# Performance work log

Hardware: AMD Instinct MI355X
Metric: run time of the kernel (lower is better)

Reference implementation:

```python
import jax, jax.numpy as jnp
import numpy as np

B, T, V, EMB, KBD, H, NF, OUT = 256, 50, 100000, 64, 64, 128, 10, 64


def setup_inputs() -> dict:
    key = jax.random.key(0)
    ks = jax.random.split(key, 18)
    s = 0.05
    f = lambda i, shape: jax.random.normal(ks[i], shape, jnp.float32) * s
    return {
        "X": jax.random.randint(ks[0], (B, T), 0, V),
        "E": f(1, (V, EMB)),
        "KBE": f(2, (V, KBD)),
        "r_matrix": f(3, (NF, KBD)),
        "gru_Wih": f(4, (3 * H, EMB)),
        "gru_Whh": f(5, (3 * H, H)),
        "gru_bih": f(6, (3 * H,)),
        "gru_bhh": f(7, (3 * H,)),
        "u_W": f(8, (KBD, H)),
        "u_b": f(9, (KBD,)),
        "ea_W": f(10, (KBD, KBD)),
        "ea_b": f(11, (KBD,)),
        "u2_W": f(12, (H, KBD + H)),
        "u2_b": f(13, (H,)),
        "m1_W": f(14, (OUT, H)),
        "m1_b": f(15, (OUT,)),
        "m2_W": f(16, (OUT, EMB + KBD)),
        "m2_b": f(17, (OUT,)),
    }


def reference(X, E, KBE, r_matrix, gru_Wih, gru_Whh, gru_bih, gru_bhh,
              u_W, u_b, ea_W, ea_b, u2_W, u2_b, m1_W, m1_b, m2_W, m2_b):
    b, t = X.shape
    nf, d = r_matrix.shape
    hdim = gru_Whh.shape[1]
    # mask row 0 of the embedding tables (padding item)
    Em = E.at[0].set(0.0)
    KBEm = KBE.at[0].set(0.0)
    Sx = Em[X]        # [B,T,EMB]
    KBx = KBEm[X]     # [B,T,KBD]

    h0 = jnp.zeros((b, hdim), Sx.dtype)
    MN0 = jnp.zeros((b, nf, d), Sx.dtype)
    ysum0 = jnp.zeros((b, m1_b.shape[0]), Sx.dtype)

    def step(carry, xs):
        h, MN, ysum = carry
        x_emb, kb = xs
        # torch GRUCell
        gi = x_emb @ gru_Wih.T + gru_bih
        gh = h @ gru_Whh.T + gru_bhh
        ir, iz, inn = jnp.split(gi, 3, axis=1)
        hr, hz, hn = jnp.split(gh, 3, axis=1)
        r = jax.nn.sigmoid(ir + hr)
        z = jax.nn.sigmoid(iz + hz)
        n = jnp.tanh(inn + r * hn)
        h = (1.0 - z) * n + z * h
        # memory write
        EA = jnp.tanh(kb @ ea_W.T + ea_b)[:, None, :] + r_matrix      # [B,NF,D]
        gate = jax.nn.sigmoid(jnp.sum(MN * EA, axis=-1, keepdims=True))  # [B,NF,1]
        MN = MN * (1.0 - gate) + EA * gate
        # memory read
        U = jnp.tanh(h @ u_W.T + u_b)                                  # [B,D]
        AW = jax.nn.softmax(U @ r_matrix.T, axis=1)                    # [B,NF]
        AC = jnp.einsum('bnd,bn->bd', MN, AW)                          # [B,D]
        Ut = jnp.tanh(jnp.concatenate([h, AC], axis=-1) @ u2_W.T + u2_b)
        y = jnp.tanh(Ut @ m1_W.T + m1_b)                               # [B,OUT]
        return (h, MN, ysum + y), None

    (h, MN, ysum), _ = jax.lax.scan(
        step, (h0, MN0, ysum0),
        (Sx.transpose(1, 0, 2), KBx.transpose(1, 0, 2)))
    y = ysum / t

    MergeE = jnp.concatenate([E, KBE], axis=1).at[0].set(0.0)  # [V, EMB+KBD]
    Sy = jnp.tanh(MergeE @ m2_W.T + m2_b)                      # [V, OUT]
    return jax.nn.log_softmax(y @ Sy.T, axis=1)                # [B, V]
```

## Files before the change

kernel.cpp:

```cpp
#include <hip/hip_runtime.h>
#include <hip/hip_bf16.h>
#include <math.h>

#define BB 256
#define TT 50
#define VV 100000
#define EMB 64
#define KBD 64
#define HH 128
#define NF 10
#define OUTD 64
#define G3H 384
#define NTILE 6250
#define DSTR 16
#define NSY 240

typedef __attribute__((ext_vector_type(8))) short sh8;
typedef __attribute__((ext_vector_type(4))) short sh4;
typedef __attribute__((ext_vector_type(4))) float f32x4;

__device__ __forceinline__ float frcp(float x){ return __builtin_amdgcn_rcpf(x); }
__device__ __forceinline__ float sigm(float x){ return frcp(1.0f+__expf(-x)); }
__device__ __forceinline__ float tanhf_(float x){ return 1.0f - 2.0f*frcp(__expf(2.0f*x)+1.0f); }
__device__ __forceinline__ short f2bs(float f){ __hip_bfloat16 h=__float2bfloat16(f); return *reinterpret_cast<short*>(&h); }
__device__ __forceinline__ sh8 ldfrag(const float* p){
  float4 a = *(const float4*)p; float4 b = *(const float4*)(p+4);
  sh8 v;
  v[0]=f2bs(a.x); v[1]=f2bs(a.y); v[2]=f2bs(a.z); v[3]=f2bs(a.w);
  v[4]=f2bs(b.x); v[5]=f2bs(b.y); v[6]=f2bs(b.z); v[7]=f2bs(b.w);
  return v;
}
__device__ __forceinline__ void barrier_lds(){
  asm volatile("s_waitcnt lgkmcnt(0)" ::: "memory");
  __builtin_amdgcn_sched_barrier(0);
  __builtin_amdgcn_s_barrier();
  __builtin_amdgcn_sched_barrier(0);
}

#define PREP 32
__global__ __launch_bounds__(512) void k_preSy(
    const int* __restrict__ X, const float* __restrict__ E, const float* __restrict__ KBE,
    const float* __restrict__ Wih, const float* __restrict__ bih, const float* __restrict__ bhh,
    const float* __restrict__ eaW, const float* __restrict__ eab,
    float* __restrict__ gi_pre, float* __restrict__ ea_pre,
    __hip_bfloat16* __restrict__ ea_bfT,
    const float* __restrict__ m2W, const float* __restrict__ m2b,
    __hip_bfloat16* __restrict__ Sy) {
  const int tid = threadIdx.x;
  const int w = tid>>6, l = tid&63, r16 = l&15, g4 = l>>4;

  if (blockIdx.x >= 400) {
    int kof = g4*8;
    sh8 bbf[4][4];
    float bias[4];
    #pragma unroll
    for (int nt=0;nt<4;nt++){
      int o = nt*16 + r16;
      bias[nt] = m2b[o];
      #pragma unroll
      for (int ks=0;ks<4;ks++) bbf[nt][ks] = ldfrag(m2W + o*128 + ks*32 + kof);
    }
    int wid = (blockIdx.x-400)*8 + w;
    for (int tile=wid; tile<NTILE; tile+=NSY*8){
      int v = tile*16 + r16;
      sh8 aa[4];
      const float* ep = E + (size_t)v*EMB + kof;
      const float* kp = KBE + (size_t)v*KBD + kof;
      aa[0] = ldfrag(ep); aa[1] = ldfrag(ep+32);
      aa[2] = ldfrag(kp); aa[3] = ldfrag(kp+32);
      if (v==0){ sh8 z={0,0,0,0,0,0,0,0}; aa[0]=z;aa[1]=z;aa[2]=z;aa[3]=z; }
      f32x4 acc[4];
      #pragma unroll
      for (int nt=0;nt<4;nt++){ f32x4 z={0.f,0.f,0.f,0.f}; acc[nt]=z; }
      #pragma unroll
      for (int nt=0;nt<4;nt++)
        #pragma unroll
        for (int ks=0;ks<4;ks++)
          acc[nt] = __builtin_amdgcn_mfma_f32_16x16x32_bf16(aa[ks],bbf[nt][ks],acc[nt],0,0,0);
      #pragma unroll
      for (int nt=0;nt<4;nt++){
        #pragma unroll
        for (int r=0;r<4;r++){
          int vv = tile*16 + g4*4 + r;
          Sy[(size_t)vv*OUTD + nt*16 + r16] = __float2bfloat16(tanhf_(acc[nt][r] + bias[nt]));
        }
      }
    }
    return;
  }

  __shared__ float xeL[PREP][68];
  __shared__ float kbL[PREP][68];
  int base = blockIdx.x * PREP;
  for (int i=tid; i<PREP*EMB; i+=512){
    int p=i>>6, k=i&63; int x = X[base+p];
    xeL[p][k] = x ? E[(size_t)x*EMB+k] : 0.0f;
    kbL[p][k] = x ? KBE[(size_t)x*KBD+k] : 0.0f;
  }
  __syncthreads();

  const int m = w>>2, nq = w&3;
  sh8 axe[2], akb[2];
  #pragma unroll
  for (int f=0;f<2;f++){
    axe[f] = ldfrag(&xeL[m*16 + r16][f*32 + g4*8]);
    akb[f] = ldfrag(&kbL[m*16 + r16][f*32 + g4*8]);
  }
  #pragma unroll
  for (int i=0;i<6;i++){
    int nt = nq*6 + i;
    int j = nt*16 + r16;
    sh8 bf0 = ldfrag(Wih + (size_t)j*EMB + g4*8);
    sh8 bf1 = ldfrag(Wih + (size_t)j*EMB + 32 + g4*8);
    f32x4 acc = {0.f,0.f,0.f,0.f};
    acc = __builtin_amdgcn_mfma_f32_16x16x32_bf16(axe[0], bf0, acc,0,0,0);
    acc = __builtin_amdgcn_mfma_f32_16x16x32_bf16(axe[1], bf1, acc,0,0,0);
    float bj = bih[j] + (j < 2*HH ? bhh[j] : 0.0f);
    #pragma unroll
    for (int r=0;r<4;r++){
      int pair = base + m*16 + g4*4 + r;
      gi_pre[(size_t)pair*G3H + j] = acc[r] + bj;
    }
  }
  {
    int d = nq*16 + r16;
    sh8 bf0 = ldfrag(eaW + (size_t)d*KBD + g4*8);
    sh8 bf1 = ldfrag(eaW + (size_t)d*KBD + 32 + g4*8);
    f32x4 acc = {0.f,0.f,0.f,0.f};
    acc = __builtin_amdgcn_mfma_f32_16x16x32_bf16(akb[0], bf0, acc,0,0,0);
    acc = __builtin_amdgcn_mfma_f32_16x16x32_bf16(akb[1], bf1, acc,0,0,0);
    float bd = eab[d];
    #pragma unroll
    for (int r=0;r<4;r++){
      int pair = base + m*16 + g4*4 + r;
      float v = tanhf(acc[r] + bd);
      ea_pre[(size_t)pair*KBD + d] = v;
      int bb = pair/TT, tt = pair - bb*TT;
      ea_bfT[((size_t)bb*64 + d)*64 + tt] = __float2bfloat16(v);
    }
  }
}

__global__ __launch_bounds__(256,2) void k_scanh(
    const float* __restrict__ gi_pre,
    const float* __restrict__ Whh, const float* __restrict__ bhh,
    const float* __restrict__ ea_pre, const float* __restrict__ rmat,
    float* __restrict__ Gg, float* __restrict__ Pg,
    __hip_bfloat16* __restrict__ h_stream) {
  const int tid = threadIdx.x;
  const int w = tid>>6, l = tid&63, r16 = l&15, g4 = l>>4;

  if (blockIdx.x >= 16) {
    const int b = (blockIdx.x-16)*4 + w;
    sh8 aa[4][2];
    #pragma unroll
    for (int i=0;i<4;i++){
      int row = i*16 + r16; if (row > TT-1) row = TT-1;
      #pragma unroll
      for (int f=0;f<2;f++)
        aa[i][f] = ldfrag(ea_pre + ((size_t)b*TT + row)*KBD + f*32 + g4*8);
    }
    sh8 rmB[2];
    #pragma unroll
    for (int f=0;f<2;f++){
      sh8 z = {0,0,0,0,0,0,0,0};
      if (r16 < NF) z = ldfrag(rmat + (size_t)r16*KBD + f*32 + g4*8);
      rmB[f] = z;
    }
    float* Gb = Gg + ((size_t)b<<12);
    #pragma unroll
    for (int i=0;i<4;i++){
      #pragma unroll
      for (int j=0;j<4;j++){
        f32x4 acc={0.f,0.f,0.f,0.f};
        #pragma unroll
        for (int f=0;f<2;f++) acc = __builtin_amdgcn_mfma_f32_16x16x32_bf16(aa[i][f], aa[j][f], acc,0,0,0);
        #pragma unroll
        for (int r=0;r<4;r++) Gb[(i*16+g4*4+r)*64 + j*16+r16] = acc[r];
      }
      f32x4 accp={0.f,0.f,0.f,0.f};
      #pragma unroll
      for (int f=0;f<2;f++) accp = __builtin_amdgcn_mfma_f32_16x16x32_bf16(aa[i][f], rmB[f], accp,0,0,0);
      #pragma unroll
      for (int r=0;r<4;r++) Pg[((size_t)b<<10) + (i*16+g4*4+r)*16 + r16] = accp[r];
    }
    return;
  }

  __shared__ __hip_bfloat16 hcat[2][16][128];
  __builtin_amdgcn_s_setprio(1);
  const int b = blockIdx.x;
  const int b0 = b*16;
  for (int i=tid;i<2*16*128;i+=256) ((short*)hcat)[i]=0;
  __syncthreads();
  const int swz = (r16&7)<<4;

  sh8 whhF[2][3][4];
  #pragma unroll
  for (int t=0;t<2;t++)
    #pragma unroll
    for (int g=0;g<3;g++){
      int chain = (w + 4*t) + 8*g;
      #pragma unroll
      for (int f=0;f<4;f++)
        whhF[t][g][f] = ldfrag(Whh + (size_t)(chain*16 + r16)*HH + f*32 + g4*8);
    }
  float4 bhn[2];
  bhn[0] = *(const float4*)(bhh + 2*HH + w*16 + g4*4);
  bhn[1] = *(const float4*)(bhh + 2*HH + (w+4)*16 + g4*4);
  float h_old[2][4] = {{0.f,0.f,0.f,0.f},{0.f,0.f,0.f,0.f}};
  const float* gi_row = gi_pre + (size_t)(b0+r16)*TT*G3H;
  __hip_bfloat16* hsb = h_stream + (size_t)b*TT*16*HH;

  int cur = 0;
  auto stepfn = [&](int s, float4 (&gi)[2][3], int cu){
    const char* hrow = (const char*)&hcat[cu][r16][0];
    sh8 hb[4];
    #pragma unroll
    for (int f=0;f<4;f++)
      hb[f] = *(const sh8*)(hrow + ((f*64 + g4*16) ^ swz));
    f32x4 aR[2], aZ[2], aN[2];
    #pragma unroll
    for (int t=0;t<2;t++){ f32x4 z={0.f,0.f,0.f,0.f}; aR[t]=z; aZ[t]=z; aN[t]=z; }
    #pragma unroll
    for (int f=0;f<4;f++){
      #pragma unroll
      for (int t=0;t<2;t++){
        aR[t] = __builtin_amdgcn_mfma_f32_16x16x32_bf16(whhF[t][0][f], hb[f], aR[t],0,0,0);
        aZ[t] = __builtin_amdgcn_mfma_f32_16x16x32_bf16(whhF[t][1][f], hb[f], aZ[t],0,0,0);
        aN[t] = __builtin_amdgcn_mfma_f32_16x16x32_bf16(whhF[t][2][f], hb[f], aN[t],0,0,0);
      }
    }
    char* hwrow = (char*)&hcat[cu^1][r16][0];
    #pragma unroll
    for (int t=0;t<2;t++){
      sh4 hp;
      #pragma unroll
      for (int r=0;r<4;r++){
        float rr = sigm(gi[t][0][r] + aR[t][r]);
        float zz = sigm(gi[t][1][r] + aZ[t][r]);
        float nn = tanhf_(gi[t][2][r] + rr*(aN[t][r] + bhn[t][r]));
        h_old[t][r] = (1.f-zz)*nn + zz*h_old[t][r];
        hp[r] = f2bs(h_old[t][r]);
      }
      *(sh4*)(hwrow + (((w+4*t)*32 + g4*8) ^ swz)) = hp;
      *(sh4*)(hsb + ((size_t)s*16 + r16)*HH + (w+4*t)*16 + g4*4) = hp;
    }
    barrier_lds();
  };

  float4 gA[2][3], gB[2][3];
  #pragma unroll
  for (int t=0;t<2;t++)
    #pragma unroll
    for (int g=0;g<3;g++)
      gA[t][g] = *(const float4*)(gi_row + g*128 + (w+4*t)*16 + g4*4);

  for (int s=0;s<TT;s+=2){
    {
      int sg = s+1;
      #pragma unroll
      for (int t=0;t<2;t++)
        #pragma unroll
        for (int g=0;g<3;g++)
          gB[t][g] = *(const float4*)(gi_row + (size_t)sg*G3H + g*128 + (w+4*t)*16 + g4*4);
      stepfn(s, gA, cur);
      cur ^= 1;
    }
    {
      int sg = (s+2<TT)? s+2 : TT-1;
      #pragma unroll
      for (int t=0;t<2;t++)
        #pragma unroll
        for (int g=0;g<3;g++)
          gA[t][g] = *(const float4*)(gi_row + (size_t)sg*G3H + g*128 + (w+4*t)*16 + g4*4);
      stepfn(s+1, gB, cur);
      cur ^= 1;
    }
  }
}

__global__ __launch_bounds__(512) void k_uaw(
    const __hip_bfloat16* __restrict__ h_stream,
    const float* __restrict__ uW, const float* __restrict__ ub,
    const float* __restrict__ rmat, float* __restrict__ aw_pre) {
  __shared__ __hip_bfloat16 u_sh[8][16][72];
  const int tid = threadIdx.x;
  const int w = tid>>6, l = tid&63, r16 = l&15, g4 = l>>4;
  sh8 uwF[4][4];
  #pragma unroll
  for (int ot=0;ot<4;ot++)
    #pragma unroll
    for (int f=0;f<4;f++)
      uwF[ot][f] = ldfrag(uW + (size_t)(ot*16+r16)*HH + f*32 + g4*8);
  sh8 rmF[2];
  #pragma unroll
  for (int f=0;f<2;f++){
    sh8 z = {0,0,0,0,0,0,0,0};
    if (r16 < NF) z = ldfrag(rmat + (size_t)r16*KBD + f*32 + g4*8);
    rmF[f] = z;
  }
  float4 ubv[4];
  #pragma unroll
  for (int ot=0;ot<4;ot++) ubv[ot] = *(const float4*)(ub + ot*16 + g4*4);

  int p0 = (blockIdx.x*8 + w)*16;
  int t = p0>>8, b0 = p0&255, fb = b0>>4;
  const __hip_bfloat16* hp = h_stream + (size_t)((fb*TT + t)*16)*HH;
  sh8 hb[4];
  #pragma unroll
  for (int f=0;f<4;f++) hb[f] = *(const sh8*)(hp + r16*HH + f*32 + g4*8);
  f32x4 u[4];
  #pragma unroll
  for (int ot=0;ot<4;ot++){ f32x4 z={0.f,0.f,0.f,0.f}; u[ot]=z; }
  #pragma unroll
  for (int ot=0;ot<4;ot++)
    #pragma unroll
    for (int f=0;f<4;f++)
      u[ot] = __builtin_amdgcn_mfma_f32_16x16x32_bf16(uwF[ot][f], hb[f], u[ot],0,0,0);
  #pragma unroll
  for (int ot=0;ot<4;ot++){
    sh4 up;
    #pragma unroll
    for (int r=0;r<4;r++) up[r] = f2bs(tanhf_(u[ot][r] + ubv[ot][r]));
    *(sh4*)&u_sh[w][l&15][ot*16 + g4*4] = up;
  }
  __syncthreads();
  sh8 uf[2];
  #pragma unroll
  for (int f=0;f<2;f++) uf[f] = *(const sh8*)&u_sh[w][r16][f*32 + g4*8];
  f32x4 al={0.f,0.f,0.f,0.f};
  #pragma unroll
  for (int f=0;f<2;f++) al = __builtin_amdgcn_mfma_f32_16x16x32_bf16(rmF[f], uf[f], al,0,0,0);
  float mx = -1e30f;
  #pragma unroll
  for (int r=0;r<4;r++){ if (g4*4+r < NF) mx = fmaxf(mx, al[r]); }
  mx = fmaxf(mx, __shfl_xor(mx,16));
  mx = fmaxf(mx, __shfl_xor(mx,32));
  float av[4]; float ssum=0.f;
  #pragma unroll
  for (int r=0;r<4;r++){ av[r] = (g4*4+r < NF) ? __expf(al[r]-mx) : 0.f; ssum += av[r]; }
  ssum += __shfl_xor(ssum,16); ssum += __shfl_xor(ssum,32);
  float inv = frcp(ssum);
  if (g4<3){
    f32x4 o = {av[0]*inv, av[1]*inv, av[2]*inv, av[3]*inv};
    *(f32x4*)&aw_pre[(size_t)(p0+r16)*16 + g4*4] = o;
  }
}

__global__ __launch_bounds__(640) void k_mnrec(
    const float* __restrict__ Gg, const float* __restrict__ Pg,
    const float* __restrict__ rmat, const float* __restrict__ aw_pre,
    __hip_bfloat16* __restrict__ Aag_bf, __hip_bfloat16* __restrict__ Bag_bf) {
  __shared__ float AagL[TT*52];
  __shared__ float BagL[TT*16];
  const int tid = threadIdx.x;
  const int n = tid>>6, l = tid&63;
  const int b = blockIdx.x;
  for (int i=tid;i<TT*52;i+=640) AagL[i]=0.f;
  for (int i=tid;i<TT*16;i+=640) BagL[i]=0.f;

  float rv = rmat[n*KBD + l];
  float R = rv*rv;
  R += __shfl_xor(R,1); R += __shfl_xor(R,2); R += __shfl_xor(R,4);
  R += __shfl_xor(R,8); R += __shfl_xor(R,16); R += __shfl_xor(R,32);

  float Pn = (l<TT)? Pg[((size_t)b<<10) + l*16 + n] : 0.f;
  const float* Gb = Gg + ((size_t)b<<12);
  float Grow = Gb[l];
  float awt = aw_pre[(size_t)(0*256+b)*16 + n];
  float d=0.f, w=0.f, q=1.f;
  __syncthreads();

  for (int t=0;t<TT;t++){
    int tn = (t+1<TT)? t+1 : TT-1;
    float GrowN = Gb[tn*64 + l];
    float awtN  = aw_pre[(size_t)(tn*256+b)*16 + n];
    float dt = __shfl(d, t);
    float g  = sigm(dt);
    float og = 1.f - g;
    float Pt = __shfl(Pn, t);
    float Ets = Grow + Pt + Pn + R;
    d = og*d + g*Ets;
    w = (l==t)? g : w*og;
    q *= og;
    if (l < TT) atomicAdd(&AagL[t*52 + l], awt*w);
    if (l == 0) BagL[t*16 + n] = awt*(1.f - q);
    Grow = GrowN; awt = awtN;
  }
  __syncthreads();
  for (int i=tid;i<4096;i+=640){
    int row=i>>6, col=i&63;
    float v = (row<TT && col<TT)? AagL[row*52+col] : 0.f;
    Aag_bf[((size_t)b<<12) + i] = __float2bfloat16(v);
  }
  for (int i=tid;i<2048;i+=640){
    int row=i>>5, col=i&31;
    float v = (row<TT && col<NF)? BagL[row*16+col] : 0.f;
    Bag_bf[((size_t)b<<11) + i] = __float2bfloat16(v);
  }
}

__global__ __launch_bounds__(512) void k_ac(
    const __hip_bfloat16* __restrict__ Aag_bf, const __hip_bfloat16* __restrict__ Bag_bf,
    const __hip_bfloat16* __restrict__ ea_bfT, const float* __restrict__ rmat,
    __hip_bfloat16* __restrict__ ac_pre) {
  const int tid = threadIdx.x;
  const int w = tid>>6, l = tid&63, r16 = l&15, g4 = l>>4;
  const int b = blockIdx.x*8 + w;
  sh8 a1[4][2], a2[4];
  #pragma unroll
  for (int i=0;i<4;i++){
    #pragma unroll
    for (int f=0;f<2;f++)
      a1[i][f] = *(const sh8*)(Aag_bf + ((size_t)b<<12) + (i*16+r16)*64 + f*32 + g4*8);
    a2[i] = *(const sh8*)(Bag_bf + ((size_t)b<<11) + (i*16+r16)*32 + g4*8);
  }
  for (int j=0;j<4;j++){
    sh8 bb1[2];
    #pragma unroll
    for (int f=0;f<2;f++)
      bb1[f] = *(const sh8*)(ea_bfT + ((size_t)b<<12) + (j*16+r16)*64 + f*32 + g4*8);
    sh8 bb2;
    #pragma unroll
    for (int c=0;c<8;c++){
      int k = g4*8 + c;
      bb2[c] = (k<NF)? f2bs(rmat[k*KBD + j*16+r16]) : (short)0;
    }
    #pragma unroll
    for (int i=0;i<4;i++){
      f32x4 acc={0.f,0.f,0.f,0.f};
      #pragma unroll
      for (int f=0;f<2;f++) acc = __builtin_amdgcn_mfma_f32_16x16x32_bf16(a1[i][f], bb1[f], acc,0,0,0);
      acc = __builtin_amdgcn_mfma_f32_16x16x32_bf16(a2[i], bb2, acc,0,0,0);
      #pragma unroll
      for (int r=0;r<4;r++){
        int t = i*16 + g4*4 + r;
        if (t < TT)
          ac_pre[((size_t)t*256 + b)*KBD + j*16 + r16] = __float2bfloat16(acc[r]);
      }
    }
  }
}

__global__ __launch_bounds__(512) void k_uty(
    const __hip_bfloat16* __restrict__ h_stream, const __hip_bfloat16* __restrict__ ac_pre,
    const float* __restrict__ u2W, const float* __restrict__ u2b,
    const float* __restrict__ m1W, const float* __restrict__ m1b,
    __hip_bfloat16* __restrict__ y_tmp) {
  __shared__ __hip_bfloat16 ut_sh[16][136];
  const int tid = threadIdx.x;
  const int w = tid>>6, l = tid&63, r16 = l&15, g4 = l>>4;
  const int t = blockIdx.x>>4, btile = blockIdx.x&15;
  const int b0 = btile*16, fb = btile;

  sh8 u2F[6];
  #pragma unroll
  for (int f=0;f<6;f++) u2F[f] = ldfrag(u2W + (size_t)(w*16+r16)*(HH+KBD) + f*32 + g4*8);
  sh8 m1F[4];
  if (w<4){
    #pragma unroll
    for (int f=0;f<4;f++) m1F[f] = ldfrag(m1W + (size_t)(w*16+r16)*HH + f*32 + g4*8);
  }
  float4 u2bv = *(const float4*)(u2b + w*16 + g4*4);

  const __hip_bfloat16* hp = h_stream + (size_t)((fb*TT + t)*16)*HH;
  const __hip_bfloat16* ap = ac_pre + ((size_t)t*256 + b0)*KBD;
  sh8 cb[6];
  #pragma unroll
  for (int f=0;f<4;f++) cb[f] = *(const sh8*)(hp + r16*HH + f*32 + g4*8);
  #pragma unroll
  for (int f=4;f<6;f++) cb[f] = *(const sh8*)(ap + r16*KBD + (f-4)*32 + g4*8);
  f32x4 at={0.f,0.f,0.f,0.f};
  #pragma unroll
  for (int f=0;f<6;f++) at = __builtin_amdgcn_mfma_f32_16x16x32_bf16(u2F[f], cb[f], at,0,0,0);
  sh4 tp;
  #pragma unroll
  for (int r=0;r<4;r++) tp[r] = f2bs(tanhf_(at[r] + u2bv[r]));
  *(sh4*)&ut_sh[r16][w*16+g4*4] = tp;
  __syncthreads();
  if (w<4){
    float4 m1bv = *(const float4*)(m1b + w*16 + g4*4);
    sh8 tb[4];
    #pragma unroll
    for (int f=0;f<4;f++) tb[f] = *(const sh8*)&ut_sh[r16][f*32+g4*8];
    f32x4 ay={0.f,0.f,0.f,0.f};
    #pragma unroll
    for (int f=0;f<4;f++) ay = __builtin_amdgcn_mfma_f32_16x16x32_bf16(m1F[f], tb[f], ay,0,0,0);
    sh4 yp;
    #pragma unroll
    for (int r=0;r<4;r++) yp[r] = f2bs(tanhf_(ay[r] + m1bv[r]));
    *(sh4*)&y_tmp[((size_t)t*256 + b0 + r16)*OUTD + w*16 + g4*4] = yp;
  }
}

__global__ __launch_bounds__(512) void k_fin(
    const __hip_bfloat16* __restrict__ y_tmp, __hip_bfloat16* __restrict__ ybf) {
  int idx = blockIdx.x*512 + threadIdx.x;
  int b = idx>>6, o = idx&63;
  float s = 0.f;
  for (int t=0;t<TT;t++) s += __bfloat162float(y_tmp[((size_t)t*256 + b)*OUTD + o]);
  ybf[(size_t)b*OUTD + o] = __float2bfloat16(s*(1.0f/TT));
}

__global__ __launch_bounds__(256) void k_logits(
    const __hip_bfloat16* __restrict__ ybf, const __hip_bfloat16* __restrict__ Sy,
    float* __restrict__ denom, float* __restrict__ out, int pass) {
  __shared__ float dsum[64];
  int lane = threadIdx.x & 63;
  int w = threadIdx.x >> 6;
  int r16 = lane & 15, g4 = lane >> 4;
  int kof = g4 * 8;
  int tbase = blockIdx.x * 16 + w * 4;
  if (pass==0){
    if (threadIdx.x<64) dsum[threadIdx.x]=0.f;
    __syncthreads();
  }
  sh8 b0[4], b1[4];
  #pragma unroll
  for (int i=0;i<4;i++){
    if (tbase + i < NTILE) {
      const __hip_bfloat16* bp = Sy + ((size_t)((tbase+i)*16 + r16))*OUTD + kof;
      b0[i] = *(const sh8*)bp;
      b1[i] = *(const sh8*)(bp + 32);
    } else {
      sh8 z = {0,0,0,0,0,0,0,0};
      b0[i]=z; b1[i]=z;
    }
  }
  int bg0 = blockIdx.y * 4;
  for (int bgi=0; bgi<4; bgi++){
    int bg = bg0 + bgi;
    const __hip_bfloat16* ap = ybf + (bg*16 + r16)*OUTD + kof;
    sh8 a0 = *(const sh8*)ap;
    sh8 a1 = *(const sh8*)(ap+32);
    if (pass == 0){
      float part[4] = {0.f,0.f,0.f,0.f};
      #pragma unroll
      for (int i=0;i<4;i++){
        if (tbase + i < NTILE){
          f32x4 acc = {0.f,0.f,0.f,0.f};
          acc = __builtin_amdgcn_mfma_f32_16x16x32_bf16(a0,b0[i],acc,0,0,0);
          acc = __builtin_amdgcn_mfma_f32_16x16x32_bf16(a1,b1[i],acc,0,0,0);
          #pragma unroll
          for (int r=0;r<4;r++) part[r] += __expf(acc[r]);
        }
      }
      #pragma unroll
      for (int r=0;r<4;r++){
        float p = part[r];
        p += __shfl_xor(p,1,16); p += __shfl_xor(p,2,16);
        p += __shfl_xor(p,4,16); p += __shfl_xor(p,8,16);
        if (r16==0) atomicAdd(&dsum[bgi*16 + g4*4 + r], p);
      }
    } else {
      float lse[4];
      #pragma unroll
      for (int r=0;r<4;r++) lse[r] = logf(denom[(size_t)(bg*16 + g4*4 + r)*DSTR]);
      #pragma unroll
      for (int i=0;i<4;i++){
        if (tbase + i < NTILE){
          f32x4 acc = {0.f,0.f,0.f,0.f};
          acc = __builtin_amdgcn_mfma_f32_16x16x32_bf16(a0,b0[i],acc,0,0,0);
          acc = __builtin_amdgcn_mfma_f32_16x16x32_bf16(a1,b1[i],acc,0,0,0);
          int vc = (tbase+i)*16 + r16;
          #pragma unroll
          for (int r=0;r<4;r++)
            out[(size_t)(bg*16 + g4*4 + r)*VV + vc] = acc[r] - lse[r];
        }
      }
    }
  }
  if (pass==0){
    __syncthreads();
    if (threadIdx.x<64)
      atomicAdd(&denom[(size_t)(bg0*16 + threadIdx.x)*DSTR], dsum[threadIdx.x]);
  }
}

extern "C" void kernel_launch(void* const* d_in, const int* in_sizes, int n_in,
                              void* d_out, int out_size, void* d_ws, size_t ws_size,
                              hipStream_t stream) {
  const int*   X    = (const int*)  d_in[0];
  const float* E    = (const float*)d_in[1];
  const float* KBE  = (const float*)d_in[2];
  const float* rmat = (const float*)d_in[3];
  const float* Wih  = (const float*)d_in[4];
  const float* Whh  = (const float*)d_in[5];
  const float* bih  = (const float*)d_in[6];
  const float* bhh  = (const float*)d_in[7];
  const float* uW   = (const float*)d_in[8];
  const float* ub   = (const float*)d_in[9];
  const float* eaW  = (const float*)d_in[10];
  const float* eab  = (const float*)d_in[11];
  const float* u2W  = (const float*)d_in[12];
  const float* u2b  = (const float*)d_in[13];
  const float* m1W  = (const float*)d_in[14];
  const float* m1b  = (const float*)d_in[15];
  const float* m2W  = (const float*)d_in[16];
  const float* m2b  = (const float*)d_in[17];
  float* outp = (float*)d_out;

  char* p = (char*)d_ws;
  float* gi_pre = (float*)p;            p += (size_t)BB*TT*G3H*4;
  float* ea_pre = (float*)p;            p += (size_t)BB*TT*KBD*4;
  float* denom  = (float*)p;            p += (size_t)BB*DSTR*4;
  float* aw_pre = (float*)p;            p += (size_t)BB*TT*16*4;
  float* Gg     = (float*)p;            p += (size_t)BB*64*64*4;
  float* Pg     = (float*)p;            p += (size_t)BB*64*16*4;
  __hip_bfloat16* h_stream = (__hip_bfloat16*)p; p += (size_t)16*TT*16*HH*2;
  __hip_bfloat16* ea_bfT = (__hip_bfloat16*)p;   p += (size_t)BB*64*64*2;
  __hip_bfloat16* Aag_bf = (__hip_bfloat16*)p;   p += (size_t)BB*64*64*2;
  __hip_bfloat16* Bag_bf = (__hip_bfloat16*)p;   p += (size_t)BB*64*32*2;
  __hip_bfloat16* ac_pre = (__hip_bfloat16*)p;   p += (size_t)BB*TT*KBD*2;
  __hip_bfloat16* y_tmp  = (__hip_bfloat16*)p;   p += (size_t)BB*TT*OUTD*2;
  __hip_bfloat16* ybf    = (__hip_bfloat16*)p;   p += (size_t)BB*OUTD*2;
  __hip_bfloat16* Sy     = (__hip_bfloat16*)p;   p += (size_t)VV*OUTD*2;

  hipMemsetAsync(denom, 0, BB*DSTR*sizeof(float), stream);
  k_preSy<<<400+NSY,512,0,stream>>>(X,E,KBE,Wih,bih,bhh,eaW,eab,gi_pre,ea_pre,ea_bfT,
                                    m2W,m2b,Sy);
  k_scanh<<<80,256,0,stream>>>(gi_pre,Whh,bhh,ea_pre,rmat,Gg,Pg,h_stream);
  k_uaw<<<100,512,0,stream>>>(h_stream,uW,ub,rmat,aw_pre);
  k_mnrec<<<256,640,0,stream>>>(Gg,Pg,rmat,aw_pre,Aag_bf,Bag_bf);
  k_ac<<<32,512,0,stream>>>(Aag_bf,Bag_bf,ea_bfT,rmat,ac_pre);
  k_uty<<<TT*16,512,0,stream>>>(h_stream,ac_pre,u2W,u2b,m1W,m1b,y_tmp);
  k_fin<<<32,512,0,stream>>>(y_tmp,ybf);
  dim3 g1((NTILE + 15)/16, 4, 1);
  k_logits<<<g1,256,0,stream>>>(ybf,Sy,denom,outp,0);
  k_logits<<<g1,256,0,stream>>>(ybf,Sy,denom,outp,1);
}
```

Measured before the change: 240.4 us.

## Fuse memory recurrence with AC matmul and move Sy computation into k_uty

Result: faster. 227.9 us (-5.2%).

```diff
diff --git a/kernel.cpp b/kernel.cpp
--- a/kernel.cpp
+++ b/kernel.cpp
@@ -38,57 +38,18 @@
 }
 
 #define PREP 32
-__global__ __launch_bounds__(512) void k_preSy(
+__global__ __launch_bounds__(512) void k_pre(
     const int* __restrict__ X, const float* __restrict__ E, const float* __restrict__ KBE,
     const float* __restrict__ Wih, const float* __restrict__ bih, const float* __restrict__ bhh,
     const float* __restrict__ eaW, const float* __restrict__ eab,
     float* __restrict__ gi_pre, float* __restrict__ ea_pre,
-    __hip_bfloat16* __restrict__ ea_bfT,
-    const float* __restrict__ m2W, const float* __restrict__ m2b,
-    __hip_bfloat16* __restrict__ Sy) {
+    __hip_bfloat16* __restrict__ ea_bfT, float* __restrict__ denom) {
   const int tid = threadIdx.x;
   const int w = tid>>6, l = tid&63, r16 = l&15, g4 = l>>4;
 
-  if (blockIdx.x >= 400) {
-    int kof = g4*8;
-    sh8 bbf[4][4];
-    float bias[4];
-    #pragma unroll
-    for (int nt=0;nt<4;nt++){
-      int o = nt*16 + r16;
-      bias[nt] = m2b[o];
-      #pragma unroll
-      for (int ks=0;ks<4;ks++) bbf[nt][ks] = ldfrag(m2W + o*128 + ks*32 + kof);
-    }
-    int wid = (blockIdx.x-400)*8 + w;
-    for (int tile=wid; tile<NTILE; tile+=NSY*8){
-      int v = tile*16 + r16;
-      sh8 aa[4];
-      const float* ep = E + (size_t)v*EMB + kof;
-      const float* kp = KBE + (size_t)v*KBD + kof;
-      aa[0] = ldfrag(ep); aa[1] = ldfrag(ep+32);
-      aa[2] = ldfrag(kp); aa[3] = ldfrag(kp+32);
-      if (v==0){ sh8 z={0,0,0,0,0,0,0,0}; aa[0]=z;aa[1]=z;aa[2]=z;aa[3]=z; }
-      f32x4 acc[4];
-      #pragma unroll
-      for (int nt=0;nt<4;nt++){ f32x4 z={0.f,0.f,0.f,0.f}; acc[nt]=z; }
-      #pragma unroll
-      for (int nt=0;nt<4;nt++)
-        #pragma unroll
-        for (int ks=0;ks<4;ks++)
-          acc[nt] = __builtin_amdgcn_mfma_f32_16x16x32_bf16(aa[ks],bbf[nt][ks],acc[nt],0,0,0);
-      #pragma unroll
-      for (int nt=0;nt<4;nt++){
-        #pragma unroll
-        for (int r=0;r<4;r++){
-          int vv = tile*16 + g4*4 + r;
-          Sy[(size_t)vv*OUTD + nt*16 + r16] = __float2bfloat16(tanhf_(acc[nt][r] + bias[nt]));
-        }
-      }
-    }
-    return;
-  }
-
+  if (blockIdx.x == 0){
+    for (int i=tid;i<BB*DSTR;i+=512) denom[i]=0.f;
+  }
   __shared__ float xeL[PREP][68];
   __shared__ float kbL[PREP][68];
   int base = blockIdx.x * PREP;
@@ -348,17 +309,18 @@
   }
 }
 
-__global__ __launch_bounds__(640) void k_mnrec(
+__global__ __launch_bounds__(640) void k_mnac(
     const float* __restrict__ Gg, const float* __restrict__ Pg,
     const float* __restrict__ rmat, const float* __restrict__ aw_pre,
-    __hip_bfloat16* __restrict__ Aag_bf, __hip_bfloat16* __restrict__ Bag_bf) {
-  __shared__ float AagL[TT*52];
-  __shared__ float BagL[TT*16];
+    const __hip_bfloat16* __restrict__ ea_bfT,
+    __hip_bfloat16* __restrict__ ac_pre) {
+  __shared__ float AagL[64*52];
+  __shared__ float BagL[64*16];
   const int tid = threadIdx.x;
   const int n = tid>>6, l = tid&63;
   const int b = blockIdx.x;
-  for (int i=tid;i<TT*52;i+=640) AagL[i]=0.f;
-  for (int i=tid;i<TT*16;i+=640) BagL[i]=0.f;
+  for (int i=tid;i<64*52;i+=640) AagL[i]=0.f;
+  for (int i=tid;i<64*16;i+=640) BagL[i]=0.f;
 
   float rv = rmat[n*KBD + l];
   float R = rv*rv;
@@ -369,7 +331,7 @@
   const float* Gb = Gg + ((size_t)b<<12);
   float Grow = Gb[l];
   float awt = aw_pre[(size_t)(0*256+b)*16 + n];
-  float d=0.f, w=0.f, q=1.f;
+  float d=0.f, w_=0.f, q=1.f;
   __syncthreads();
 
   for (int t=0;t<TT;t++){
@@ -382,41 +344,26 @@
     float Pt = __shfl(Pn, t);
     float Ets = Grow + Pt + Pn + R;
     d = og*d + g*Ets;
-    w = (l==t)? g : w*og;
+    w_ = (l==t)? g : w_*og;
     q *= og;
-    if (l < TT) atomicAdd(&AagL[t*52 + l], awt*w);
+    if (l < TT) atomicAdd(&AagL[t*52 + l], awt*w_);
     if (l == 0) BagL[t*16 + n] = awt*(1.f - q);
     Grow = GrowN; awt = awtN;
   }
   __syncthreads();
-  for (int i=tid;i<4096;i+=640){
-    int row=i>>6, col=i&63;
-    float v = (row<TT && col<TT)? AagL[row*52+col] : 0.f;
-    Aag_bf[((size_t)b<<12) + i] = __float2bfloat16(v);
-  }
-  for (int i=tid;i<2048;i+=640){
-    int row=i>>5, col=i&31;
-    float v = (row<TT && col<NF)? BagL[row*16+col] : 0.f;
-    Bag_bf[((size_t)b<<11) + i] = __float2bfloat16(v);
-  }
-}
-
-__global__ __launch_bounds__(512) void k_ac(
-    const __hip_bfloat16* __restrict__ Aag_bf, const __hip_bfloat16* __restrict__ Bag_bf,
-    const __hip_bfloat16* __restrict__ ea_bfT, const float* __restrict__ rmat,
-    __hip_bfloat16* __restrict__ ac_pre) {
-  const int tid = threadIdx.x;
-  const int w = tid>>6, l = tid&63, r16 = l&15, g4 = l>>4;
-  const int b = blockIdx.x*8 + w;
-  sh8 a1[4][2], a2[4];
-  #pragma unroll
-  for (int i=0;i<4;i++){
-    #pragma unroll
-    for (int f=0;f<2;f++)
-      a1[i][f] = *(const sh8*)(Aag_bf + ((size_t)b<<12) + (i*16+r16)*64 + f*32 + g4*8);
-    a2[i] = *(const sh8*)(Bag_bf + ((size_t)b<<11) + (i*16+r16)*32 + g4*8);
-  }
-  for (int j=0;j<4;j++){
+
+  const int w = n, r16 = l&15, g4 = l>>4;
+  if (w < 4){
+    sh8 a1[4][2], a2[4];
+    #pragma unroll
+    for (int i=0;i<4;i++){
+      int row = i*16 + r16;
+      #pragma unroll
+      for (int f=0;f<2;f++) a1[i][f] = ldfrag(&AagL[row*52 + f*32 + g4*8]);
+      a2[i] = ldfrag(&BagL[row*16 + ((g4*8) & 15)]);
+      if (g4 >= 2){ sh8 z={0,0,0,0,0,0,0,0}; a2[i]=z; }
+    }
+    int j = w;
     sh8 bb1[2];
     #pragma unroll
     for (int f=0;f<2;f++)
@@ -447,10 +394,54 @@
     const __hip_bfloat16* __restrict__ h_stream, const __hip_bfloat16* __restrict__ ac_pre,
     const float* __restrict__ u2W, const float* __restrict__ u2b,
     const float* __restrict__ m1W, const float* __restrict__ m1b,
-    __hip_bfloat16* __restrict__ y_tmp) {
+    __hip_bfloat16* __restrict__ y_tmp,
+    const float* __restrict__ E, const float* __restrict__ KBE,
+    const float* __restrict__ m2W, const float* __restrict__ m2b,
+    __hip_bfloat16* __restrict__ Sy) {
   __shared__ __hip_bfloat16 ut_sh[16][136];
   const int tid = threadIdx.x;
   const int w = tid>>6, l = tid&63, r16 = l&15, g4 = l>>4;
+
+  if (blockIdx.x >= 800) {
+    int kof = g4*8;
+    sh8 bbf[4][4];
+    float bias[4];
+    #pragma unroll
+    for (int nt=0;nt<4;nt++){
+      int o = nt*16 + r16;
+      bias[nt] = m2b[o];
+      #pragma unroll
+      for (int ks=0;ks<4;ks++) bbf[nt][ks] = ldfrag(m2W + o*128 + ks*32 + kof);
+    }
+    int wid = (blockIdx.x-800)*8 + w;
+    for (int tile=wid; tile<NTILE; tile+=NSY*8){
+      int v = tile*16 + r16;
+      sh8 aa[4];
+      const float* ep = E + (size_t)v*EMB + kof;
+      const float* kp = KBE + (size_t)v*KBD + kof;
+      aa[0] = ldfrag(ep); aa[1] = ldfrag(ep+32);
+      aa[2] = ldfrag(kp); aa[3] = ldfrag(kp+32);
+      if (v==0){ sh8 z={0,0,0,0,0,0,0,0}; aa[0]=z;aa[1]=z;aa[2]=z;aa[3]=z; }
+      f32x4 acc[4];
+      #pragma unroll
+      for (int nt=0;nt<4;nt++){ f32x4 z={0.f,0.f,0.f,0.f}; acc[nt]=z; }
+      #pragma unroll
+      for (int nt=0;nt<4;nt++)
+        #pragma unroll
+        for (int ks=0;ks<4;ks++)
+          acc[nt] = __builtin_amdgcn_mfma_f32_16x16x32_bf16(aa[ks],bbf[nt][ks],acc[nt],0,0,0);
+      #pragma unroll
+      for (int nt=0;nt<4;nt++){
+        #pragma unroll
+        for (int r=0;r<4;r++){
+          int vv = tile*16 + g4*4 + r;
+          Sy[(size_t)vv*OUTD + nt*16 + r16] = __float2bfloat16(tanhf_(acc[nt][r] + bias[nt]));
+        }
+      }
+    }
+    return;
+  }
+
   const int t = blockIdx.x>>4, btile = blockIdx.x&15;
   const int b0 = btile*16, fb = btile;
 
@@ -610,21 +601,17 @@
   float* Pg     = (float*)p;            p += (size_t)BB*64*16*4;
   __hip_bfloat16* h_stream = (__hip_bfloat16*)p; p += (size_t)16*TT*16*HH*2;
   __hip_bfloat16* ea_bfT = (__hip_bfloat16*)p;   p += (size_t)BB*64*64*2;
-  __hip_bfloat16* Aag_bf = (__hip_bfloat16*)p;   p += (size_t)BB*64*64*2;
-  __hip_bfloat16* Bag_bf = (__hip_bfloat16*)p;   p += (size_t)BB*64*32*2;
   __hip_bfloat16* ac_pre = (__hip_bfloat16*)p;   p += (size_t)BB*TT*KBD*2;
   __hip_bfloat16* y_tmp  = (__hip_bfloat16*)p;   p += (size_t)BB*TT*OUTD*2;
   __hip_bfloat16* ybf    = (__hip_bfloat16*)p;   p += (size_t)BB*OUTD*2;
   __hip_bfloat16* Sy     = (__hip_bfloat16*)p;   p += (size_t)VV*OUTD*2;
 
-  hipMemsetAsync(denom, 0, BB*DSTR*sizeof(float), stream);
-  k_preSy<<<400+NSY,512,0,stream>>>(X,E,KBE,Wih,bih,bhh,eaW,eab,gi_pre,ea_pre,ea_bfT,
-                                    m2W,m2b,Sy);
+  k_pre<<<400,512,0,stream>>>(X,E,KBE,Wih,bih,bhh,eaW,eab,gi_pre,ea_pre,ea_bfT,denom);
   k_scanh<<<80,256,0,stream>>>(gi_pre,Whh,bhh,ea_pre,rmat,Gg,Pg,h_stream);
   k_uaw<<<100,512,0,stream>>>(h_stream,uW,ub,rmat,aw_pre);
-  k_mnrec<<<256,640,0,stream>>>(Gg,Pg,rmat,aw_pre,Aag_bf,Bag_bf);
-  k_ac<<<32,512,0,stream>>>(Aag_bf,Bag_bf,ea_bfT,rmat,ac_pre);
-  k_uty<<<TT*16,512,0,stream>>>(h_stream,ac_pre,u2W,u2b,m1W,m1b,y_tmp);
+  k_mnac<<<256,640,0,stream>>>(Gg,Pg,rmat,aw_pre,ea_bfT,ac_pre);
+  k_uty<<<800+NSY,512,0,stream>>>(h_stream,ac_pre,u2W,u2b,m1W,m1b,y_tmp,
+                                  E,KBE,m2W,m2b,Sy);
   k_fin<<<32,512,0,stream>>>(y_tmp,ybf);
   dim3 g1((NTILE + 15)/16, 4, 1);
   k_logits<<<g1,256,0,stream>>>(ybf,Sy,denom,outp,0);
```
